# Kernel tuning notes

Hardware: AMD Instinct MI355X
Metric: run time of the kernel (lower is better)

## Reference

```python
import jax, jax.numpy as jnp
import numpy as np

B, T, D, H, L, O = 256, 512, 64, 256, 2, 4


def _lstm_layer(x_tbd, W_ih, W_hh, b_ih, b_hh):
    """x_tbd: (T, B, D_in) -> hidden sequence (T, B, H). PyTorch gate order i,f,g,o."""
    Bb = x_tbd.shape[1]
    Hh = W_hh.shape[1]
    b = b_ih + b_hh
    # precompute input projections for all timesteps in one GEMM
    xW = jnp.einsum('tbd,gd->tbg', x_tbd, W_ih) + b  # (T, B, 4H)

    def step(carry, xw_t):
        h, c = carry
        gates = xw_t + h @ W_hh.T
        i, f, g, o = jnp.split(gates, 4, axis=-1)
        i = jax.nn.sigmoid(i)
        f = jax.nn.sigmoid(f)
        g = jnp.tanh(g)
        o = jax.nn.sigmoid(o)
        c = f * c + i * g
        h = o * jnp.tanh(c)
        return (h, c), h

    init = (jnp.zeros((Bb, Hh), x_tbd.dtype), jnp.zeros((Bb, Hh), x_tbd.dtype))
    _, hs = jax.lax.scan(step, init, xW)
    return hs


def setup_inputs() -> dict:
    key = jax.random.key(0)
    ks = jax.random.split(key, 11)
    s = 1.0 / np.sqrt(H)  # PyTorch LSTM init scale
    inp = {
        'x': jax.random.normal(ks[0], (B, T, D), dtype=jnp.float32),
        'W_ih0': jax.random.uniform(ks[1], (4 * H, D), minval=-s, maxval=s, dtype=jnp.float32),
        'W_hh0': jax.random.uniform(ks[2], (4 * H, H), minval=-s, maxval=s, dtype=jnp.float32),
        'b_ih0': jax.random.uniform(ks[3], (4 * H,), minval=-s, maxval=s, dtype=jnp.float32),
        'b_hh0': jax.random.uniform(ks[4], (4 * H,), minval=-s, maxval=s, dtype=jnp.float32),
        'W_ih1': jax.random.uniform(ks[5], (4 * H, H), minval=-s, maxval=s, dtype=jnp.float32),
        'W_hh1': jax.random.uniform(ks[6], (4 * H, H), minval=-s, maxval=s, dtype=jnp.float32),
        'b_ih1': jax.random.uniform(ks[7], (4 * H,), minval=-s, maxval=s, dtype=jnp.float32),
        'b_hh1': jax.random.uniform(ks[8], (4 * H,), minval=-s, maxval=s, dtype=jnp.float32),
        'fc_W': jax.random.uniform(ks[9], (O, H), minval=-s, maxval=s, dtype=jnp.float32),
        'fc_b': jax.random.uniform(ks[10], (O,), minval=-s, maxval=s, dtype=jnp.float32),
    }
    return inp


def reference(x, W_ih0, W_hh0, b_ih0, b_hh0, W_ih1, W_hh1, b_ih1, b_hh1, fc_W, fc_b):
    xt = jnp.transpose(x, (1, 0, 2))            # (T, B, D), batch_first -> time-major
    h1 = _lstm_layer(xt, W_ih0, W_hh0, b_ih0, b_hh0)   # (T, B, H)
    h2 = _lstm_layer(h1, W_ih1, W_hh1, b_ih1, b_hh1)   # (T, B, H)
    last = h2[-1]                                # out[:, -1, :] in batch_first layout
    return last @ fc_W.T + fc_b                  # (B, O)
```

## Files before the change

### kernel.cpp

```cpp
#include <hip/hip_runtime.h>


#define TT 512
#define HH 256
#define DD 64

typedef __attribute__((ext_vector_type(2))) _Float16 h2t;
typedef __attribute__((ext_vector_type(8))) _Float16 f16x8;
typedef __attribute__((ext_vector_type(4))) float f32x4;
typedef unsigned long long u64;
typedef unsigned u32;

__device__ __forceinline__ u32 pkh(float x, float y) {
    h2t h; h.x = (_Float16)x; h.y = (_Float16)y;
    return __builtin_bit_cast(u32, h);
}
__device__ __forceinline__ float sigf(float x) { return 1.f / (1.f + __expf(-x)); }
__device__ __forceinline__ float tanhf_(float x) {
    float e = __expf(2.f * x);
    return 1.f - 2.f / (e + 1.f);
}
__device__ __forceinline__ f16x8 ld8(const float* p) {
    float4 u = ((const float4*)p)[0];
    float4 v = ((const float4*)p)[1];
    f16x8 r = {(_Float16)u.x, (_Float16)u.y, (_Float16)u.z, (_Float16)u.w,
               (_Float16)v.x, (_Float16)v.y, (_Float16)v.z, (_Float16)v.w};
    return r;
}
__device__ __forceinline__ u32 ld32(const u32* p) {
    return __hip_atomic_load(p, __ATOMIC_RELAXED, __HIP_MEMORY_SCOPE_AGENT);
}
__device__ __forceinline__ void st32(u32* p, u32 v) {
    __hip_atomic_store(p, v, __ATOMIC_RELAXED, __HIP_MEMORY_SCOPE_AGENT);
}
__device__ __forceinline__ u64 ld64(const u64* p) {
    return __hip_atomic_load(p, __ATOMIC_RELAXED, __HIP_MEMORY_SCOPE_AGENT);
}
__device__ __forceinline__ void st64(u64* p, u64 v) {
    __hip_atomic_store(p, v, __ATOMIC_RELAXED, __HIP_MEMORY_SCOPE_AGENT);
}

__global__ __launch_bounds__(512, 2) void lstm_persist(
    const float* __restrict__ x,
    const float* __restrict__ Wih0, const float* __restrict__ Whh0,
    const float* __restrict__ bih0, const float* __restrict__ bhh0,
    const float* __restrict__ Wih1, const float* __restrict__ Whh1,
    const float* __restrict__ bih1, const float* __restrict__ bhh1,
    const float* __restrict__ fcW, const float* __restrict__ fcb,
    float* __restrict__ out,
    u64* h0ring, u64* h1ring, u32* cflagsA)
{
    __shared__ __align__(16) _Float16 sB[9216];
    __shared__ __align__(16) float part2[2][8][276];

    const int tid  = threadIdx.x;
    const int g    = blockIdx.x & 31;
    const int role = blockIdx.x >> 5;
    const bool isL1 = role >= 4;
    const int q = role & 3;
    const int batch0 = g * 8;
    u64* ring0 = h0ring + (size_t)g * 4096;
    u64* ring1 = h1ring + (size_t)g * 4096;
    u32* cflag = cflagsA + (size_t)g * 16;

    const int lane = tid & 63, w = tid >> 6;
    const int mw = w & 3, kh = w >> 2;
    const int bcol = lane & 15, kc = lane >> 4;

    const int R0 = mw * 256 + 64 * q + (lane & 15);
    const int R1 = R0 + 16, R2 = R0 + 32, R3 = R0 + 48;

#define DECL_TI(ti) f16x8 A##ti##_0={},A##ti##_1={},A##ti##_2={},A##ti##_3={}, \
                          A##ti##_4={},A##ti##_5={},A##ti##_6={},A##ti##_7={};
    DECL_TI(0) DECL_TI(1) DECL_TI(2) DECL_TI(3)
#undef DECL_TI

    if (isL1) {
#define LDA1(ti,j) { int k_ = (kh*8+(j))*32 + kc*8;                          \
        A##ti##_##j = ld8(k_ < 256 ? Wih1 + (size_t)R##ti*256 + k_           \
                                   : Whh1 + (size_t)R##ti*256 + (k_-256)); }
#define LDA1T(ti) LDA1(ti,0) LDA1(ti,1) LDA1(ti,2) LDA1(ti,3) \
                  LDA1(ti,4) LDA1(ti,5) LDA1(ti,6) LDA1(ti,7)
        LDA1T(0) LDA1T(1) LDA1T(2) LDA1T(3)
#undef LDA1T
#undef LDA1
    } else {
#define LDA0(ti,j) { int k_ = (kh*5+(j))*32 + kc*8;                          \
        A##ti##_##j = ld8(k_ < 64 ? Wih0 + (size_t)R##ti*64 + k_             \
                                  : Whh0 + (size_t)R##ti*256 + (k_-64)); }
#define LDA0T(ti) LDA0(ti,0) LDA0(ti,1) LDA0(ti,2) LDA0(ti,3) LDA0(ti,4)
        LDA0T(0) LDA0T(1) LDA0T(2) LDA0T(3)
#undef LDA0T
#undef LDA0
    }

    const float* bA = isL1 ? bih1 : bih0;
    const float* bB = isL1 ? bhh1 : bhh0;
    const float bz0 = bA[      64*q + lane] + bB[      64*q + lane];
    const float bz1 = bA[256 + 64*q + lane] + bB[256 + 64*q + lane];
    const float bz2 = bA[512 + 64*q + lane] + bB[512 + 64*q + lane];
    const float bz3 = bA[768 + 64*q + lane] + bB[768 + 64*q + lane];
    float cst = 0.f;

    u32* const sBu = (u32*)sB;
    for (int i = tid; i < 4608; i += 512) sBu[i] = 0;
    __syncthreads();

    if (!isL1 && tid >= 256 && tid < 384) {
        int t2 = tid - 256, j = t2 >> 4, c = t2 & 15;
        float4 v = ((const float4*)(x + ((size_t)(batch0 + j) * TT) * DD))[c];
        int bidx = (c >> 1) * 72 + j * 4 + 2 * (c & 1);
        sBu[bidx]     = pkh(v.x, v.y);
        sBu[bidx + 1] = pkh(v.z, v.w);
    }

    for (int s = 0; s <= TT; ++s) {
        __syncthreads();
        if (tid == 0) st32(&cflag[role], (u32)(s + 1));

        const bool act_ = isL1 ? (s >= 1) : (s < TT);
        const int  snx  = s + 1;
        const bool stg0 = (!isL1) && (snx < TT);
        const bool stg1 = isL1 && (snx <= TT);

        u32 cpre = 0u;
        if (act_ && lane < 8) cpre = ld32(&cflag[lane]);
        float4 xr;
        const bool doX = stg0 && (tid >= 256) && (tid < 384);
        if (doX) {
            int t2 = tid - 256, j = t2 >> 4, c = t2 & 15;
            xr = ((const float4*)(x + ((size_t)(batch0 + j) * TT + snx) * DD))[c];
        }

        if (act_) {
            f32x4 C0 = {0,0,0,0}, C1 = {0,0,0,0}, C2 = {0,0,0,0}, C3 = {0,0,0,0};
#define MST(j, ktb) { const f16x8 Bf = *(const f16x8*)(sB + (((ktb)+(j))*4 + kc)*144 + bcol*8); \
            C0 = __builtin_amdgcn_mfma_f32_16x16x32_f16(A0_##j, Bf, C0, 0,0,0); \
            C1 = __builtin_amdgcn_mfma_f32_16x16x32_f16(A1_##j, Bf, C1, 0,0,0); \
            C2 = __builtin_amdgcn_mfma_f32_16x16x32_f16(A2_##j, Bf, C2, 0,0,0); \
            C3 = __builtin_amdgcn_mfma_f32_16x16x32_f16(A3_##j, Bf, C3, 0,0,0); }
            if (isL1) {
                const int ktb = kh * 8;
                MST(0,ktb) MST(1,ktb) MST(2,ktb) MST(3,ktb)
                MST(4,ktb) MST(5,ktb) MST(6,ktb) MST(7,ktb)
            } else {
                const int ktb = kh * 5;
                MST(0,ktb) MST(1,ktb) MST(2,ktb) MST(3,ktb) MST(4,ktb)
            }
#undef MST
            if (bcol < 8) {
                *(f32x4*)&part2[kh][bcol][mw*64 +  0 + kc*4] = C0;
                *(f32x4*)&part2[kh][bcol][mw*64 + 16 + kc*4] = C1;
                *(f32x4*)&part2[kh][bcol][mw*64 + 32 + kc*4] = C2;
                *(f32x4*)&part2[kh][bcol][mw*64 + 48 + kc*4] = C3;
            }
        }
        __syncthreads();

        if (act_) {
            float s0 = part2[0][w][      lane] + part2[1][w][      lane] + bz0;
            float s1 = part2[0][w][ 64 + lane] + part2[1][w][ 64 + lane] + bz1;
            float s2 = part2[0][w][128 + lane] + part2[1][w][128 + lane] + bz2;
            float s3 = part2[0][w][192 + lane] + part2[1][w][192 + lane] + bz3;
            float fi = sigf(s0), ff = sigf(s1), fg = tanhf_(s2), fo = sigf(s3);
            cst = ff * cst + fi * fg;
            float h = fo * tanhf_(cst);
            float hn = __shfl_down(h, 1);
            u32 hw = pkh(h, hn);

            const int tgt = s - 2;
            while (!__all(lane >= 8 || (int)cpre >= tgt)) {
                __builtin_amdgcn_s_sleep(1);
                if (lane < 8) cpre = ld32(&cflag[lane]);
            }
            if (!(lane & 1)) {
                u64 v = ((u64)(u32)(s + 1) << 32) | (u64)hw;
                u64* dst = (isL1 ? ring1 + (size_t)((s - 1) & 3) * 1024
                                 : ring0 + (size_t)(s & 3) * 1024)
                           + q * 256 + w * 32 + (lane >> 1);
                st64(dst, v);
            }
        }

        if (stg0 || stg1) {
            const int n0  = tid & 127;
            const int jj0 = tid >> 7, jj1 = 4 + jj0;
            const u64* b0 = ring0 + (size_t)((snx - 1) & 3) * 1024
                            + ((n0 >> 5) << 8) + (n0 & 31);
            const u64* a00 = b0 + jj0 * 32;
            const u64* a01 = b0 + jj1 * 32;
            u64 v00, v01, v10 = 0, v11 = 0;
            const u64 *a10 = nullptr, *a11 = nullptr;
            if (isL1) {
                const u64* b1 = ring1 + (size_t)((snx + 2) & 3) * 1024
                                + ((n0 >> 5) << 8) + (n0 & 31);
                a10 = b1 + jj0 * 32; a11 = b1 + jj1 * 32;
                v00 = ld64(a00); v01 = ld64(a01);
                v10 = ld64(a10); v11 = ld64(a11);
            } else {
                v00 = ld64(a00); v01 = ld64(a01);
            }
            const u32 e0 = (u32)snx;
            const u32 e1 = (snx >= 2) ? (u32)snx : 0u;
            for (;;) {
                bool k0 = ((u32)(v00 >> 32) == e0);
                bool k1 = ((u32)(v01 >> 32) == e0);
                bool k2 = !isL1 || ((u32)(v10 >> 32) == e1);
                bool k3 = !isL1 || ((u32)(v11 >> 32) == e1);
                if (k0 & k1 & k2 & k3) break;
                if (!k0) v00 = ld64(a00);
                if (!k1) v01 = ld64(a01);
                if (isL1) {
                    if (!k2) v10 = ld64(a10);
                    if (!k3) v11 = ld64(a11);
                }
            }
            const int cb0 = isL1 ? 0 : 8;
            sBu[(cb0 + (n0 >> 2)) * 72 + jj0 * 4 + (n0 & 3)] = (u32)v00;
            sBu[(cb0 + (n0 >> 2)) * 72 + jj1 * 4 + (n0 & 3)] = (u32)v01;
            if (isL1) {
                sBu[(32 + (n0 >> 2)) * 72 + jj0 * 4 + (n0 & 3)] = (u32)v10;
                sBu[(32 + (n0 >> 2)) * 72 + jj1 * 4 + (n0 & 3)] = (u32)v11;
            }
            if (doX) {
                int t2 = tid - 256, j = t2 >> 4, c = t2 & 15;
                int bidx = (c >> 1) * 72 + j * 4 + 2 * (c & 1);
                sBu[bidx]     = pkh(xr.x, xr.y);
                sBu[bidx + 1] = pkh(xr.z, xr.w);
            }
        }
    }

    if (isL1 && q == 0) {
        const u32 ef = (u32)(TT + 1);
        const int n0  = tid & 127;
        const int jj0 = tid >> 7, jj1 = 4 + jj0;
        const u64* b = ring1 + 3 * 1024 + ((n0 >> 5) << 8) + (n0 & 31);
        const u64* a0 = b + jj0 * 32;
        const u64* a1 = b + jj1 * 32;
        u64 v0 = ld64(a0), v1 = ld64(a1);
        for (;;) {
            bool k0 = ((u32)(v0 >> 32) == ef), k1 = ((u32)(v1 >> 32) == ef);
            if (k0 & k1) break;
            if (!k0) v0 = ld64(a0);
            if (!k1) v1 = ld64(a1);
        }
        sBu[jj0 * 128 + n0] = (u32)v0;
        sBu[jj1 * 128 + n0] = (u32)v1;
        __syncthreads();
        const int j = tid >> 6, l2 = tid & 63;
        const int o = l2 >> 4, kk = l2 & 15;
        float ssum = 0.f;
#pragma unroll
        for (int m = 0; m < 16; ++m) {
            int k = kk * 16 + m;
            ssum += (float)sB[j * 256 + k] * fcW[o * HH + k];
        }
#pragma unroll
        for (int off = 8; off; off >>= 1) ssum += __shfl_down(ssum, off);
        if (kk == 0) out[(batch0 + j) * 4 + o] = ssum + fcb[o];
    }
}

extern "C" void kernel_launch(void* const* d_in, const int* in_sizes, int n_in,
                              void* d_out, int out_size, void* d_ws, size_t ws_size,
                              hipStream_t stream)
{
    (void)in_sizes; (void)n_in; (void)out_size; (void)ws_size;
    const float* x    = (const float*)d_in[0];
    const float* Wih0 = (const float*)d_in[1];
    const float* Whh0 = (const float*)d_in[2];
    const float* bih0 = (const float*)d_in[3];
    const float* bhh0 = (const float*)d_in[4];
    const float* Wih1 = (const float*)d_in[5];
    const float* Whh1 = (const float*)d_in[6];
    const float* bih1 = (const float*)d_in[7];
    const float* bhh1 = (const float*)d_in[8];
    const float* fcW  = (const float*)d_in[9];
    const float* fcb  = (const float*)d_in[10];
    float* out = (float*)d_out;

    u64* h0ring = (u64*)d_ws;
    u64* h1ring = (u64*)((char*)d_ws + 1048576);
    u32* cflags = (u32*)((char*)d_ws + 2097152);

    hipMemsetAsync(d_ws, 0, 2097152 + 2048, stream);

    lstm_persist<<<dim3(256), dim3(512), 0, stream>>>(
        x, Wih0, Whh0, bih0, bhh0, Wih1, Whh1, bih1, bhh1, fcW, fcb, out,
        h0ring, h1ring, cflags);
}
```

Before: 1.319 ms.

## Process two batch groups per block and interleave their MFMA and activation phases

Each persistent block now handles two 8-sample batch groups (A and B) instead of one, which halves the grid to 128 blocks. The MFMA for group B is issued right after group A's activation, so matrix work and transcendental math from the two groups can overlap, and the register-resident weights are reused across both. The cost is that each block does twice the serial work per step on half as many CUs, plus an extra barrier and twice the shared memory. Ring polling and the final FC are widened to cover both groups.

```diff
diff --git a/kernel.cpp b/kernel.cpp
--- a/kernel.cpp
+++ b/kernel.cpp
@@ -50,18 +50,23 @@
     float* __restrict__ out,
     u64* h0ring, u64* h1ring, u32* cflagsA)
 {
-    __shared__ __align__(16) _Float16 sB[9216];
-    __shared__ __align__(16) float part2[2][8][276];
+    __shared__ __align__(16) _Float16 sBA[9216];
+    __shared__ __align__(16) _Float16 sBB[9216];
+    __shared__ __align__(16) float p2A[2][8][276];
+    __shared__ __align__(16) float p2B[2][8][276];
 
     const int tid  = threadIdx.x;
-    const int g    = blockIdx.x & 31;
-    const int role = blockIdx.x >> 5;
+    const int sg   = blockIdx.x & 15;
+    const int role = blockIdx.x >> 4;
     const bool isL1 = role >= 4;
     const int q = role & 3;
-    const int batch0 = g * 8;
-    u64* ring0 = h0ring + (size_t)g * 4096;
-    u64* ring1 = h1ring + (size_t)g * 4096;
-    u32* cflag = cflagsA + (size_t)g * 16;
+    const int gA = sg * 2, gB = sg * 2 + 1;
+    const int batch0A = gA * 8, batch0B = gB * 8;
+    u64* rA0 = h0ring + (size_t)gA * 4096;
+    u64* rA1 = h1ring + (size_t)gA * 4096;
+    u64* rB0 = h0ring + (size_t)gB * 4096;
+    u64* rB1 = h1ring + (size_t)gB * 4096;
+    u32* cflag = cflagsA + (size_t)sg * 16;
 
     const int lane = tid & 63, w = tid >> 6;
     const int mw = w & 3, kh = w >> 2;
@@ -100,19 +105,58 @@
     const float bz1 = bA[256 + 64*q + lane] + bB[256 + 64*q + lane];
     const float bz2 = bA[512 + 64*q + lane] + bB[512 + 64*q + lane];
     const float bz3 = bA[768 + 64*q + lane] + bB[768 + 64*q + lane];
-    float cst = 0.f;
-
-    u32* const sBu = (u32*)sB;
-    for (int i = tid; i < 4608; i += 512) sBu[i] = 0;
+    float cstA = 0.f, cstB = 0.f;
+
+    u32* const sBuA = (u32*)sBA;
+    u32* const sBuB = (u32*)sBB;
+    for (int i = tid; i < 4608; i += 512) { sBuA[i] = 0; sBuB[i] = 0; }
     __syncthreads();
 
-    if (!isL1 && tid >= 256 && tid < 384) {
-        int t2 = tid - 256, j = t2 >> 4, c = t2 & 15;
-        float4 v = ((const float4*)(x + ((size_t)(batch0 + j) * TT) * DD))[c];
+    if (!isL1 && tid >= 256) {
+        const bool aA = tid < 384;
+        int t2 = aA ? tid - 256 : tid - 384;
+        int j = t2 >> 4, c = t2 & 15;
+        float4 v = ((const float4*)(
+            x + ((size_t)((aA ? batch0A : batch0B) + j) * TT) * DD))[c];
+        u32* du = aA ? sBuA : sBuB;
         int bidx = (c >> 1) * 72 + j * 4 + 2 * (c & 1);
-        sBu[bidx]     = pkh(v.x, v.y);
-        sBu[bidx + 1] = pkh(v.z, v.w);
+        du[bidx] = pkh(v.x, v.y); du[bidx + 1] = pkh(v.z, v.w);
     }
+
+#define MST(j, ktb, SBP) { const f16x8 Bf = *(const f16x8*)((SBP) + (((ktb)+(j))*4 + kc)*144 + bcol*8); \
+    C0 = __builtin_amdgcn_mfma_f32_16x16x32_f16(A0_##j, Bf, C0, 0,0,0); \
+    C1 = __builtin_amdgcn_mfma_f32_16x16x32_f16(A1_##j, Bf, C1, 0,0,0); \
+    C2 = __builtin_amdgcn_mfma_f32_16x16x32_f16(A2_##j, Bf, C2, 0,0,0); \
+    C3 = __builtin_amdgcn_mfma_f32_16x16x32_f16(A3_##j, Bf, C3, 0,0,0); }
+#define MFMA_STREAM(SBP, P2) do {                                            \
+    f32x4 C0={0,0,0,0},C1={0,0,0,0},C2={0,0,0,0},C3={0,0,0,0};               \
+    if (isL1) { const int ktb = kh * 8;                                      \
+        MST(0,ktb,SBP) MST(1,ktb,SBP) MST(2,ktb,SBP) MST(3,ktb,SBP)          \
+        MST(4,ktb,SBP) MST(5,ktb,SBP) MST(6,ktb,SBP) MST(7,ktb,SBP)          \
+    } else { const int ktb = kh * 5;                                         \
+        MST(0,ktb,SBP) MST(1,ktb,SBP) MST(2,ktb,SBP) MST(3,ktb,SBP)          \
+        MST(4,ktb,SBP) }                                                     \
+    if (bcol < 8) {                                                          \
+        *(f32x4*)&P2[kh][bcol][mw*64 +  0 + kc*4] = C0;                      \
+        *(f32x4*)&P2[kh][bcol][mw*64 + 16 + kc*4] = C1;                      \
+        *(f32x4*)&P2[kh][bcol][mw*64 + 32 + kc*4] = C2;                      \
+        *(f32x4*)&P2[kh][bcol][mw*64 + 48 + kc*4] = C3;                      \
+    } } while (0)
+
+#define ACT_STREAM(P2, CST, RBASE) do {                                      \
+    float s0 = P2[0][w][      lane] + P2[1][w][      lane] + bz0;            \
+    float s1 = P2[0][w][ 64 + lane] + P2[1][w][ 64 + lane] + bz1;            \
+    float s2 = P2[0][w][128 + lane] + P2[1][w][128 + lane] + bz2;            \
+    float s3 = P2[0][w][192 + lane] + P2[1][w][192 + lane] + bz3;            \
+    float fi = sigf(s0), ff = sigf(s1), fg = tanhf_(s2), fo = sigf(s3);      \
+    CST = ff * CST + fi * fg;                                                \
+    float h = fo * tanhf_(CST);                                              \
+    float hn = __shfl_down(h, 1);                                            \
+    u32 hw = pkh(h, hn);                                                     \
+    if (!(lane & 1)) {                                                       \
+        u64 v = ((u64)(u32)(s + 1) << 32) | (u64)hw;                         \
+        st64((RBASE) + q * 256 + w * 32 + (lane >> 1), v);                   \
+    } } while (0)
 
     for (int s = 0; s <= TT; ++s) {
         __syncthreads();
@@ -126,139 +170,141 @@
         u32 cpre = 0u;
         if (act_ && lane < 8) cpre = ld32(&cflag[lane]);
         float4 xr;
-        const bool doX = stg0 && (tid >= 256) && (tid < 384);
-        if (doX) {
-            int t2 = tid - 256, j = t2 >> 4, c = t2 & 15;
-            xr = ((const float4*)(x + ((size_t)(batch0 + j) * TT + snx) * DD))[c];
-        }
+        const bool doXA = stg0 && tid >= 256 && tid < 384;
+        const bool doXB = stg0 && tid >= 384;
+        if (doXA || doXB) {
+            int t2 = doXA ? tid - 256 : tid - 384;
+            int j = t2 >> 4, c = t2 & 15;
+            int b0x = doXA ? batch0A : batch0B;
+            xr = ((const float4*)(x + ((size_t)(b0x + j) * TT + snx) * DD))[c];
+        }
+
+        if (act_) MFMA_STREAM(sBA, p2A);
+        __syncthreads();
 
         if (act_) {
-            f32x4 C0 = {0,0,0,0}, C1 = {0,0,0,0}, C2 = {0,0,0,0}, C3 = {0,0,0,0};
-#define MST(j, ktb) { const f16x8 Bf = *(const f16x8*)(sB + (((ktb)+(j))*4 + kc)*144 + bcol*8); \
-            C0 = __builtin_amdgcn_mfma_f32_16x16x32_f16(A0_##j, Bf, C0, 0,0,0); \
-            C1 = __builtin_amdgcn_mfma_f32_16x16x32_f16(A1_##j, Bf, C1, 0,0,0); \
-            C2 = __builtin_amdgcn_mfma_f32_16x16x32_f16(A2_##j, Bf, C2, 0,0,0); \
-            C3 = __builtin_amdgcn_mfma_f32_16x16x32_f16(A3_##j, Bf, C3, 0,0,0); }
-            if (isL1) {
-                const int ktb = kh * 8;
-                MST(0,ktb) MST(1,ktb) MST(2,ktb) MST(3,ktb)
-                MST(4,ktb) MST(5,ktb) MST(6,ktb) MST(7,ktb)
-            } else {
-                const int ktb = kh * 5;
-                MST(0,ktb) MST(1,ktb) MST(2,ktb) MST(3,ktb) MST(4,ktb)
-            }
-#undef MST
-            if (bcol < 8) {
-                *(f32x4*)&part2[kh][bcol][mw*64 +  0 + kc*4] = C0;
-                *(f32x4*)&part2[kh][bcol][mw*64 + 16 + kc*4] = C1;
-                *(f32x4*)&part2[kh][bcol][mw*64 + 32 + kc*4] = C2;
-                *(f32x4*)&part2[kh][bcol][mw*64 + 48 + kc*4] = C3;
-            }
-        }
-        __syncthreads();
-
-        if (act_) {
-            float s0 = part2[0][w][      lane] + part2[1][w][      lane] + bz0;
-            float s1 = part2[0][w][ 64 + lane] + part2[1][w][ 64 + lane] + bz1;
-            float s2 = part2[0][w][128 + lane] + part2[1][w][128 + lane] + bz2;
-            float s3 = part2[0][w][192 + lane] + part2[1][w][192 + lane] + bz3;
-            float fi = sigf(s0), ff = sigf(s1), fg = tanhf_(s2), fo = sigf(s3);
-            cst = ff * cst + fi * fg;
-            float h = fo * tanhf_(cst);
-            float hn = __shfl_down(h, 1);
-            u32 hw = pkh(h, hn);
-
             const int tgt = s - 2;
             while (!__all(lane >= 8 || (int)cpre >= tgt)) {
                 __builtin_amdgcn_s_sleep(1);
                 if (lane < 8) cpre = ld32(&cflag[lane]);
             }
-            if (!(lane & 1)) {
-                u64 v = ((u64)(u32)(s + 1) << 32) | (u64)hw;
-                u64* dst = (isL1 ? ring1 + (size_t)((s - 1) & 3) * 1024
-                                 : ring0 + (size_t)(s & 3) * 1024)
-                           + q * 256 + w * 32 + (lane >> 1);
-                st64(dst, v);
-            }
+            ACT_STREAM(p2A, cstA,
+                       (isL1 ? rA1 + (size_t)((s - 1) & 3) * 1024
+                             : rA0 + (size_t)(s & 3) * 1024));
+            MFMA_STREAM(sBB, p2B);
+        }
+        __syncthreads();
+
+        if (act_) {
+            ACT_STREAM(p2B, cstB,
+                       (isL1 ? rB1 + (size_t)((s - 1) & 3) * 1024
+                             : rB0 + (size_t)(s & 3) * 1024));
         }
 
         if (stg0 || stg1) {
             const int n0  = tid & 127;
             const int jj0 = tid >> 7, jj1 = 4 + jj0;
-            const u64* b0 = ring0 + (size_t)((snx - 1) & 3) * 1024
-                            + ((n0 >> 5) << 8) + (n0 & 31);
-            const u64* a00 = b0 + jj0 * 32;
-            const u64* a01 = b0 + jj1 * 32;
-            u64 v00, v01, v10 = 0, v11 = 0;
-            const u64 *a10 = nullptr, *a11 = nullptr;
+            const size_t qoff = (size_t)((n0 >> 5) << 8) + (n0 & 31);
+            const u64* bA0 = rA0 + (size_t)((snx - 1) & 3) * 1024 + qoff;
+            const u64* bB0 = rB0 + (size_t)((snx - 1) & 3) * 1024 + qoff;
+            const u64 *aA00 = bA0 + jj0*32, *aA01 = bA0 + jj1*32;
+            const u64 *aB00 = bB0 + jj0*32, *aB01 = bB0 + jj1*32;
+            u64 vA00 = ld64(aA00), vA01 = ld64(aA01);
+            u64 vB00 = ld64(aB00), vB01 = ld64(aB01);
+            u64 vA10 = 0, vA11 = 0, vB10 = 0, vB11 = 0;
+            const u64 *aA10 = nullptr, *aA11 = nullptr,
+                      *aB10 = nullptr, *aB11 = nullptr;
             if (isL1) {
-                const u64* b1 = ring1 + (size_t)((snx + 2) & 3) * 1024
-                                + ((n0 >> 5) << 8) + (n0 & 31);
-                a10 = b1 + jj0 * 32; a11 = b1 + jj1 * 32;
-                v00 = ld64(a00); v01 = ld64(a01);
-                v10 = ld64(a10); v11 = ld64(a11);
-            } else {
-                v00 = ld64(a00); v01 = ld64(a01);
+                const u64* bA1 = rA1 + (size_t)((snx + 2) & 3) * 1024 + qoff;
+                const u64* bB1 = rB1 + (size_t)((snx + 2) & 3) * 1024 + qoff;
+                aA10 = bA1 + jj0*32; aA11 = bA1 + jj1*32;
+                aB10 = bB1 + jj0*32; aB11 = bB1 + jj1*32;
+                vA10 = ld64(aA10); vA11 = ld64(aA11);
+                vB10 = ld64(aB10); vB11 = ld64(aB11);
             }
             const u32 e0 = (u32)snx;
             const u32 e1 = (snx >= 2) ? (u32)snx : 0u;
             for (;;) {
-                bool k0 = ((u32)(v00 >> 32) == e0);
-                bool k1 = ((u32)(v01 >> 32) == e0);
-                bool k2 = !isL1 || ((u32)(v10 >> 32) == e1);
-                bool k3 = !isL1 || ((u32)(v11 >> 32) == e1);
-                if (k0 & k1 & k2 & k3) break;
-                if (!k0) v00 = ld64(a00);
-                if (!k1) v01 = ld64(a01);
+                bool kA0 = ((u32)(vA00 >> 32) == e0);
+                bool kA1 = ((u32)(vA01 >> 32) == e0);
+                bool kB0 = ((u32)(vB00 >> 32) == e0);
+                bool kB1 = ((u32)(vB01 >> 32) == e0);
+                bool kA2 = !isL1 || ((u32)(vA10 >> 32) == e1);
+                bool kA3 = !isL1 || ((u32)(vA11 >> 32) == e1);
+                bool kB2 = !isL1 || ((u32)(vB10 >> 32) == e1);
+                bool kB3 = !isL1 || ((u32)(vB11 >> 32) == e1);
+                if (kA0 & kA1 & kB0 & kB1 & kA2 & kA3 & kB2 & kB3) break;
+                if (!kA0) vA00 = ld64(aA00);
+                if (!kA1) vA01 = ld64(aA01);
+                if (!kB0) vB00 = ld64(aB00);
+                if (!kB1) vB01 = ld64(aB01);
                 if (isL1) {
-                    if (!k2) v10 = ld64(a10);
-                    if (!k3) v11 = ld64(a11);
+                    if (!kA2) vA10 = ld64(aA10);
+                    if (!kA3) vA11 = ld64(aA11);
+                    if (!kB2) vB10 = ld64(aB10);
+                    if (!kB3) vB11 = ld64(aB11);
                 }
             }
             const int cb0 = isL1 ? 0 : 8;
-            sBu[(cb0 + (n0 >> 2)) * 72 + jj0 * 4 + (n0 & 3)] = (u32)v00;
-            sBu[(cb0 + (n0 >> 2)) * 72 + jj1 * 4 + (n0 & 3)] = (u32)v01;
+            const int oj0 = (cb0 + (n0 >> 2)) * 72 + jj0 * 4 + (n0 & 3);
+            const int oj1 = (cb0 + (n0 >> 2)) * 72 + jj1 * 4 + (n0 & 3);
+            sBuA[oj0] = (u32)vA00; sBuA[oj1] = (u32)vA01;
+            sBuB[oj0] = (u32)vB00; sBuB[oj1] = (u32)vB01;
             if (isL1) {
-                sBu[(32 + (n0 >> 2)) * 72 + jj0 * 4 + (n0 & 3)] = (u32)v10;
-                sBu[(32 + (n0 >> 2)) * 72 + jj1 * 4 + (n0 & 3)] = (u32)v11;
-            }
-            if (doX) {
-                int t2 = tid - 256, j = t2 >> 4, c = t2 & 15;
+                const int pj0 = (32 + (n0 >> 2)) * 72 + jj0 * 4 + (n0 & 3);
+                const int pj1 = (32 + (n0 >> 2)) * 72 + jj1 * 4 + (n0 & 3);
+                sBuA[pj0] = (u32)vA10; sBuA[pj1] = (u32)vA11;
+                sBuB[pj0] = (u32)vB10; sBuB[pj1] = (u32)vB11;
+            }
+            if (doXA || doXB) {
+                int t2 = doXA ? tid - 256 : tid - 384;
+                int j = t2 >> 4, c = t2 & 15;
+                u32* du = doXA ? sBuA : sBuB;
                 int bidx = (c >> 1) * 72 + j * 4 + 2 * (c & 1);
-                sBu[bidx]     = pkh(xr.x, xr.y);
-                sBu[bidx + 1] = pkh(xr.z, xr.w);
+                du[bidx]     = pkh(xr.x, xr.y);
+                du[bidx + 1] = pkh(xr.z, xr.w);
             }
         }
     }
+#undef MST
+#undef MFMA_STREAM
+#undef ACT_STREAM
 
     if (isL1 && q == 0) {
         const u32 ef = (u32)(TT + 1);
         const int n0  = tid & 127;
         const int jj0 = tid >> 7, jj1 = 4 + jj0;
-        const u64* b = ring1 + 3 * 1024 + ((n0 >> 5) << 8) + (n0 & 31);
-        const u64* a0 = b + jj0 * 32;
-        const u64* a1 = b + jj1 * 32;
-        u64 v0 = ld64(a0), v1 = ld64(a1);
+        const size_t qoff = (size_t)((n0 >> 5) << 8) + (n0 & 31);
+        const u64* bA = rA1 + 3 * 1024 + qoff;
+        const u64* bB = rB1 + 3 * 1024 + qoff;
+        const u64 *a0 = bA + jj0*32, *a1 = bA + jj1*32;
+        const u64 *a2 = bB + jj0*32, *a3 = bB + jj1*32;
+        u64 v0 = ld64(a0), v1 = ld64(a1), v2 = ld64(a2), v3 = ld64(a3);
         for (;;) {
             bool k0 = ((u32)(v0 >> 32) == ef), k1 = ((u32)(v1 >> 32) == ef);
-            if (k0 & k1) break;
-            if (!k0) v0 = ld64(a0);
-            if (!k1) v1 = ld64(a1);
-        }
-        sBu[jj0 * 128 + n0] = (u32)v0;
-        sBu[jj1 * 128 + n0] = (u32)v1;
+            bool k2 = ((u32)(v2 >> 32) == ef), k3 = ((u32)(v3 >> 32) == ef);
+            if (k0 & k1 & k2 & k3) break;
+            if (!k0) v0 = ld64(a0);  if (!k1) v1 = ld64(a1);
+            if (!k2) v2 = ld64(a2);  if (!k3) v3 = ld64(a3);
+        }
+        sBuA[jj0 * 128 + n0] = (u32)v0;
+        sBuA[jj1 * 128 + n0] = (u32)v1;
+        sBuB[jj0 * 128 + n0] = (u32)v2;
+        sBuB[jj1 * 128 + n0] = (u32)v3;
         __syncthreads();
-        const int j = tid >> 6, l2 = tid & 63;
-        const int o = l2 >> 4, kk = l2 & 15;
+        const int j = tid >> 5;
+        const int l2 = tid & 31, o = l2 >> 3, kk = l2 & 7;
+        const _Float16* hsrc = (j < 8) ? (sBA + j * 256) : (sBB + (j - 8) * 256);
         float ssum = 0.f;
 #pragma unroll
-        for (int m = 0; m < 16; ++m) {
-            int k = kk * 16 + m;
-            ssum += (float)sB[j * 256 + k] * fcW[o * HH + k];
-        }
-#pragma unroll
-        for (int off = 8; off; off >>= 1) ssum += __shfl_down(ssum, off);
-        if (kk == 0) out[(batch0 + j) * 4 + o] = ssum + fcb[o];
+        for (int m = 0; m < 32; ++m) {
+            int k = kk * 32 + m;
+            ssum += (float)hsrc[k] * fcW[o * HH + k];
+        }
+        ssum += __shfl_down(ssum, 4);
+        ssum += __shfl_down(ssum, 2);
+        ssum += __shfl_down(ssum, 1);
+        if (kk == 0) out[(sg * 16 + j) * 4 + o] = ssum + fcb[o];
     }
 }
 
@@ -286,7 +332,7 @@
 
     hipMemsetAsync(d_ws, 0, 2097152 + 2048, stream);
 
-    lstm_persist<<<dim3(256), dim3(512), 0, stream>>>(
+    lstm_persist<<<dim3(128), dim3(512), 0, stream>>>(
         x, Wih0, Whh0, bih0, bhh0, Wih1, Whh1, bih1, bhh1, fcW, fcb, out,
         h0ring, h1ring, cflags);
 }
```

Result: slower. 1.835 ms (+39.1%).

## Split recurrent matmul around the h-wait and deepen rings to eight slots

Applied to the files above, without the earlier changes.

Each step now first stages the inputs that are already available: the layer-0 h or x for layer 1, and x for layer 0. It issues the matmul slices over those inputs, then waits for the own-layer recurrent h and finishes the remaining MFMAs. Layer 1 is shifted to lag two steps, and the ring buffers grow from 4 to 8 slots so the producer back-pressure check can be relaxed to s-5. The aim is to hide cross-block polling latency behind useful MFMA work on the critical recurrent path. The cost is an extra barrier per step, an uneven MFMA split across waves, and double the workspace and memset size.

```diff
diff --git a/kernel.cpp b/kernel.cpp
--- a/kernel.cpp
+++ b/kernel.cpp
@@ -59,8 +59,8 @@
     const bool isL1 = role >= 4;
     const int q = role & 3;
     const int batch0 = g * 8;
-    u64* ring0 = h0ring + (size_t)g * 4096;
-    u64* ring1 = h1ring + (size_t)g * 4096;
+    u64* ring0 = h0ring + (size_t)g * 8192;
+    u64* ring1 = h1ring + (size_t)g * 8192;
     u32* cflag = cflagsA + (size_t)g * 16;
 
     const int lane = tid & 63, w = tid >> 6;
@@ -106,48 +106,105 @@
     for (int i = tid; i < 4608; i += 512) sBu[i] = 0;
     __syncthreads();
 
-    if (!isL1 && tid >= 256 && tid < 384) {
+    const int n0 = tid & 127;
+    const int jj0 = tid >> 7, jj1 = 4 + jj0;
+    const size_t qoff = (size_t)((n0 >> 5) << 8) + (n0 & 31);
+
+    const bool xduty = (!isL1) && (tid >= 256) && (tid < 384);
+    float4 xr = {0, 0, 0, 0};
+    if (xduty) {
         int t2 = tid - 256, j = t2 >> 4, c = t2 & 15;
-        float4 v = ((const float4*)(x + ((size_t)(batch0 + j) * TT) * DD))[c];
-        int bidx = (c >> 1) * 72 + j * 4 + 2 * (c & 1);
-        sBu[bidx]     = pkh(v.x, v.y);
-        sBu[bidx + 1] = pkh(v.z, v.w);
+        xr = ((const float4*)(x + (size_t)(batch0 + j) * TT * DD))[c];
     }
 
-    for (int s = 0; s <= TT; ++s) {
+#define MST(j, ktb) { const f16x8 Bf = *(const f16x8*)(sB + (((ktb)+(j))*4 + kc)*144 + bcol*8); \
+    C0 = __builtin_amdgcn_mfma_f32_16x16x32_f16(A0_##j, Bf, C0, 0,0,0); \
+    C1 = __builtin_amdgcn_mfma_f32_16x16x32_f16(A1_##j, Bf, C1, 0,0,0); \
+    C2 = __builtin_amdgcn_mfma_f32_16x16x32_f16(A2_##j, Bf, C2, 0,0,0); \
+    C3 = __builtin_amdgcn_mfma_f32_16x16x32_f16(A3_##j, Bf, C3, 0,0,0); }
+
+    for (int s = 0; s <= TT + 1; ++s) {
+        const bool actL = isL1 ? (s >= 2) : (s < TT);
+
+        __syncthreads();
+
+        u64 f0 = 0, f1 = 0;
+        const u64 *af0 = nullptr, *af1 = nullptr;
+        u32 efr = 0;
+        if (actL) {
+            if (isL1) {
+                const u64* b1 = ring1 + (size_t)((s - 3) & 7) * 1024 + qoff;
+                af0 = b1 + jj0 * 32; af1 = b1 + jj1 * 32;
+                efr = (u32)(s - 2);
+            } else {
+                const u64* b0 = ring0 + (size_t)((s - 1) & 7) * 1024 + qoff;
+                af0 = b0 + jj0 * 32; af1 = b0 + jj1 * 32;
+                efr = (u32)s;
+            }
+            f0 = ld64(af0); f1 = ld64(af1);
+        }
+
+        if (actL) {
+            if (isL1) {
+                const u64* b0 = ring0 + (size_t)((s - 2) & 7) * 1024 + qoff;
+                const u64 *a0 = b0 + jj0 * 32, *a1 = b0 + jj1 * 32;
+                u64 v0 = ld64(a0), v1 = ld64(a1);
+                const u32 eo = (u32)(s - 1);
+                for (;;) {
+                    bool k0 = ((u32)(v0 >> 32) == eo), k1 = ((u32)(v1 >> 32) == eo);
+                    if (k0 & k1) break;
+                    if (!k0) v0 = ld64(a0);
+                    if (!k1) v1 = ld64(a1);
+                }
+                sBu[(n0 >> 2) * 72 + jj0 * 4 + (n0 & 3)] = (u32)v0;
+                sBu[(n0 >> 2) * 72 + jj1 * 4 + (n0 & 3)] = (u32)v1;
+            } else if (xduty) {
+                int t2 = tid - 256, j = t2 >> 4, c = t2 & 15;
+                int bidx = (c >> 1) * 72 + j * 4 + 2 * (c & 1);
+                sBu[bidx]     = pkh(xr.x, xr.y);
+                sBu[bidx + 1] = pkh(xr.z, xr.w);
+            }
+        }
+        __syncthreads();
+
+        f32x4 C0 = {0,0,0,0}, C1 = {0,0,0,0}, C2 = {0,0,0,0}, C3 = {0,0,0,0};
+        if (actL) {
+            if (isL1) {
+                if (kh == 0) { MST(0,0) MST(1,0) MST(2,0) MST(3,0)
+                               MST(4,0) MST(5,0) MST(6,0) MST(7,0) }
+            } else {
+                if (kh == 0) { MST(0,0) MST(1,0) }
+            }
+        }
+
+        if (actL) {
+            for (;;) {
+                bool k0 = ((u32)(f0 >> 32) == efr), k1 = ((u32)(f1 >> 32) == efr);
+                if (k0 & k1) break;
+                if (!k0) f0 = ld64(af0);
+                if (!k1) f1 = ld64(af1);
+            }
+            const int cb = isL1 ? 32 : 8;
+            sBu[(cb + (n0 >> 2)) * 72 + jj0 * 4 + (n0 & 3)] = (u32)f0;
+            sBu[(cb + (n0 >> 2)) * 72 + jj1 * 4 + (n0 & 3)] = (u32)f1;
+        }
         __syncthreads();
         if (tid == 0) st32(&cflag[role], (u32)(s + 1));
-
-        const bool act_ = isL1 ? (s >= 1) : (s < TT);
-        const int  snx  = s + 1;
-        const bool stg0 = (!isL1) && (snx < TT);
-        const bool stg1 = isL1 && (snx <= TT);
-
-        u32 cpre = 0u;
-        if (act_ && lane < 8) cpre = ld32(&cflag[lane]);
-        float4 xr;
-        const bool doX = stg0 && (tid >= 256) && (tid < 384);
-        if (doX) {
+        u32 cpre = 0;
+        if (actL && lane < 8) cpre = ld32(&cflag[lane]);
+        if (xduty && (s + 1 < TT)) {
             int t2 = tid - 256, j = t2 >> 4, c = t2 & 15;
-            xr = ((const float4*)(x + ((size_t)(batch0 + j) * TT + snx) * DD))[c];
-        }
-
-        if (act_) {
-            f32x4 C0 = {0,0,0,0}, C1 = {0,0,0,0}, C2 = {0,0,0,0}, C3 = {0,0,0,0};
-#define MST(j, ktb) { const f16x8 Bf = *(const f16x8*)(sB + (((ktb)+(j))*4 + kc)*144 + bcol*8); \
-            C0 = __builtin_amdgcn_mfma_f32_16x16x32_f16(A0_##j, Bf, C0, 0,0,0); \
-            C1 = __builtin_amdgcn_mfma_f32_16x16x32_f16(A1_##j, Bf, C1, 0,0,0); \
-            C2 = __builtin_amdgcn_mfma_f32_16x16x32_f16(A2_##j, Bf, C2, 0,0,0); \
-            C3 = __builtin_amdgcn_mfma_f32_16x16x32_f16(A3_##j, Bf, C3, 0,0,0); }
+            xr = ((const float4*)(x + ((size_t)(batch0 + j) * TT + (s + 1)) * DD))[c];
+        }
+
+        if (actL) {
             if (isL1) {
-                const int ktb = kh * 8;
-                MST(0,ktb) MST(1,ktb) MST(2,ktb) MST(3,ktb)
-                MST(4,ktb) MST(5,ktb) MST(6,ktb) MST(7,ktb)
+                if (kh == 1) { MST(0,8) MST(1,8) MST(2,8) MST(3,8)
+                               MST(4,8) MST(5,8) MST(6,8) MST(7,8) }
             } else {
-                const int ktb = kh * 5;
-                MST(0,ktb) MST(1,ktb) MST(2,ktb) MST(3,ktb) MST(4,ktb)
-            }
-#undef MST
+                if (kh == 0) { MST(2,0) MST(3,0) MST(4,0) }
+                else         { MST(0,5) MST(1,5) MST(2,5) MST(3,5) MST(4,5) }
+            }
             if (bcol < 8) {
                 *(f32x4*)&part2[kh][bcol][mw*64 +  0 + kc*4] = C0;
                 *(f32x4*)&part2[kh][bcol][mw*64 + 16 + kc*4] = C1;
@@ -157,7 +214,14 @@
         }
         __syncthreads();
 
-        if (act_) {
+        if (actL) {
+            const int tgt = s - 5;
+            if (tgt > 0) {
+                while (!__all(lane >= 8 || (int)cpre >= tgt)) {
+                    __builtin_amdgcn_s_sleep(1);
+                    if (lane < 8) cpre = ld32(&cflag[lane]);
+                }
+            }
             float s0 = part2[0][w][      lane] + part2[1][w][      lane] + bz0;
             float s1 = part2[0][w][ 64 + lane] + part2[1][w][ 64 + lane] + bz1;
             float s2 = part2[0][w][128 + lane] + part2[1][w][128 + lane] + bz2;
@@ -167,75 +231,20 @@
             float h = fo * tanhf_(cst);
             float hn = __shfl_down(h, 1);
             u32 hw = pkh(h, hn);
-
-            const int tgt = s - 2;
-            while (!__all(lane >= 8 || (int)cpre >= tgt)) {
-                __builtin_amdgcn_s_sleep(1);
-                if (lane < 8) cpre = ld32(&cflag[lane]);
-            }
             if (!(lane & 1)) {
-                u64 v = ((u64)(u32)(s + 1) << 32) | (u64)hw;
-                u64* dst = (isL1 ? ring1 + (size_t)((s - 1) & 3) * 1024
-                                 : ring0 + (size_t)(s & 3) * 1024)
+                u64 v = ((u64)(u32)(isL1 ? (s - 1) : (s + 1)) << 32) | (u64)hw;
+                u64* dst = (isL1 ? ring1 + (size_t)((s - 2) & 7) * 1024
+                                 : ring0 + (size_t)(s & 7) * 1024)
                            + q * 256 + w * 32 + (lane >> 1);
                 st64(dst, v);
             }
         }
-
-        if (stg0 || stg1) {
-            const int n0  = tid & 127;
-            const int jj0 = tid >> 7, jj1 = 4 + jj0;
-            const u64* b0 = ring0 + (size_t)((snx - 1) & 3) * 1024
-                            + ((n0 >> 5) << 8) + (n0 & 31);
-            const u64* a00 = b0 + jj0 * 32;
-            const u64* a01 = b0 + jj1 * 32;
-            u64 v00, v01, v10 = 0, v11 = 0;
-            const u64 *a10 = nullptr, *a11 = nullptr;
-            if (isL1) {
-                const u64* b1 = ring1 + (size_t)((snx + 2) & 3) * 1024
-                                + ((n0 >> 5) << 8) + (n0 & 31);
-                a10 = b1 + jj0 * 32; a11 = b1 + jj1 * 32;
-                v00 = ld64(a00); v01 = ld64(a01);
-                v10 = ld64(a10); v11 = ld64(a11);
-            } else {
-                v00 = ld64(a00); v01 = ld64(a01);
-            }
-            const u32 e0 = (u32)snx;
-            const u32 e1 = (snx >= 2) ? (u32)snx : 0u;
-            for (;;) {
-                bool k0 = ((u32)(v00 >> 32) == e0);
-                bool k1 = ((u32)(v01 >> 32) == e0);
-                bool k2 = !isL1 || ((u32)(v10 >> 32) == e1);
-                bool k3 = !isL1 || ((u32)(v11 >> 32) == e1);
-                if (k0 & k1 & k2 & k3) break;
-                if (!k0) v00 = ld64(a00);
-                if (!k1) v01 = ld64(a01);
-                if (isL1) {
-                    if (!k2) v10 = ld64(a10);
-                    if (!k3) v11 = ld64(a11);
-                }
-            }
-            const int cb0 = isL1 ? 0 : 8;
-            sBu[(cb0 + (n0 >> 2)) * 72 + jj0 * 4 + (n0 & 3)] = (u32)v00;
-            sBu[(cb0 + (n0 >> 2)) * 72 + jj1 * 4 + (n0 & 3)] = (u32)v01;
-            if (isL1) {
-                sBu[(32 + (n0 >> 2)) * 72 + jj0 * 4 + (n0 & 3)] = (u32)v10;
-                sBu[(32 + (n0 >> 2)) * 72 + jj1 * 4 + (n0 & 3)] = (u32)v11;
-            }
-            if (doX) {
-                int t2 = tid - 256, j = t2 >> 4, c = t2 & 15;
-                int bidx = (c >> 1) * 72 + j * 4 + 2 * (c & 1);
-                sBu[bidx]     = pkh(xr.x, xr.y);
-                sBu[bidx + 1] = pkh(xr.z, xr.w);
-            }
-        }
     }
+#undef MST
 
     if (isL1 && q == 0) {
-        const u32 ef = (u32)(TT + 1);
-        const int n0  = tid & 127;
-        const int jj0 = tid >> 7, jj1 = 4 + jj0;
-        const u64* b = ring1 + 3 * 1024 + ((n0 >> 5) << 8) + (n0 & 31);
+        const u32 ef = (u32)TT;
+        const u64* b = ring1 + (size_t)7 * 1024 + qoff;
         const u64* a0 = b + jj0 * 32;
         const u64* a1 = b + jj1 * 32;
         u64 v0 = ld64(a0), v1 = ld64(a1);
@@ -281,10 +290,10 @@
     float* out = (float*)d_out;
 
     u64* h0ring = (u64*)d_ws;
-    u64* h1ring = (u64*)((char*)d_ws + 1048576);
-    u32* cflags = (u32*)((char*)d_ws + 2097152);
-
-    hipMemsetAsync(d_ws, 0, 2097152 + 2048, stream);
+    u64* h1ring = (u64*)((char*)d_ws + 2097152);
+    u32* cflags = (u32*)((char*)d_ws + 4194304);
+
+    hipMemsetAsync(d_ws, 0, 4194304 + 2048, stream);
 
     lstm_persist<<<dim3(256), dim3(512), 0, stream>>>(
         x, Wih0, Whh0, bih0, bhh0, Wih1, Whh1, bih1, bhh1, fcW, fcb, out,
```

New measurement: 1.723 ms. +30.6%, slower.
